# Optimization experiments

Measured on AMD Instinct MI355X. Metric: run time of the kernel, lower is better.

The kernel has to match this reference:

```python
import jax, jax.numpy as jnp
import numpy as np

B, T, E, H = 8, 1024, 1024, 16
D = E // H  # head_dim = 64


def setup_inputs() -> dict:
    key = jax.random.key(0)
    ks = jax.random.split(key, 11)
    s = 1.0 / np.sqrt(E)
    inp = {
        'query': jax.random.normal(ks[0], (B, T, E), jnp.float32),
        'key': jax.random.normal(ks[1], (B, T, E), jnp.float32),
        'value': jax.random.normal(ks[2], (B, T, E), jnp.float32),
        'Wq': jax.random.uniform(ks[3], (E, E), jnp.float32, -s, s),
        'bq': jax.random.uniform(ks[4], (E,), jnp.float32, -s, s),
        'Wk': jax.random.uniform(ks[5], (E, E), jnp.float32, -s, s),
        'bk': jax.random.uniform(ks[6], (E,), jnp.float32, -s, s),
        'Wv': jax.random.uniform(ks[7], (E, E), jnp.float32, -s, s),
        'bv': jax.random.uniform(ks[8], (E,), jnp.float32, -s, s),
        'Wo': jax.random.uniform(ks[9], (E, E), jnp.float32, -s, s),
        'bo': jax.random.uniform(ks[10], (E,), jnp.float32, -s, s),
    }
    return inp


def reference(query, key, value, Wq, bq, Wk, bk, Wv, bv, Wo, bo):
    scale = np.sqrt(D).astype(np.float32)
    # projections: Linear applies x @ W.T + b (torch convention); W shape (out,in)
    q = (query @ Wq.T + bq).reshape(B, T, H, D).transpose(0, 2, 1, 3)  # (B,H,Tq,D)
    k = (key @ Wk.T + bk).reshape(B, T, H, D).transpose(0, 2, 1, 3)    # (B,H,Tk,D)
    v = (value @ Wv.T + bv).reshape(B, T, H, D).transpose(0, 2, 1, 3)  # (B,H,Tk,D)
    scores = jnp.einsum('bhqd,bhkd->bhqk', q, k) / scale
    attn = jax.nn.softmax(scores, axis=-1)  # dropout = identity (eval)
    out = jnp.einsum('bhqk,bhkd->bhqd', attn, v)
    out = out.transpose(0, 2, 1, 3).reshape(B, T, E)
    return out @ Wo.T + bo
```

## Files before the change

### kernel.cpp

```cpp
#include <hip/hip_runtime.h>
#include <stdint.h>

#define BB 8
#define TT 1024
#define EE 1024
#define HH 16
#define DD 64

#define L2E8 0.18033688011112042f

typedef __attribute__((ext_vector_type(8))) __bf16 bf16x8;
typedef __attribute__((ext_vector_type(4))) float f32x4;
typedef __attribute__((ext_vector_type(4))) unsigned short ushort4v;
typedef __attribute__((ext_vector_type(4))) unsigned int uint4v;

__device__ __forceinline__ unsigned short f2bf(float f) {
  unsigned int u = __float_as_uint(f);
  u += 0x7fffu + ((u >> 16) & 1u);
  return (unsigned short)(u >> 16);
}

__device__ __forceinline__ unsigned int pk2t(float a, float b) {
  return __builtin_amdgcn_perm(__float_as_uint(b) + 0x8000u,
                               __float_as_uint(a) + 0x8000u, 0x07060302u);
}

__device__ __forceinline__ f32x4 mfma_16x16x32(bf16x8 a, bf16x8 b, f32x4 c) {
  return __builtin_amdgcn_mfma_f32_16x16x32_bf16(a, b, c, 0, 0, 0);
}

__device__ __forceinline__ void async_ld16(const unsigned short* g, unsigned short* l) {
  __builtin_amdgcn_global_load_lds(
      (const __attribute__((address_space(1))) void*)g,
      (__attribute__((address_space(3))) void*)l, 16, 0, 0);
}

__global__ __launch_bounds__(256) void cast_all(
    const float* __restrict__ xq, const float* __restrict__ xk, const float* __restrict__ xv,
    const float* __restrict__ wq, const float* __restrict__ wk,
    const float* __restrict__ wv, const float* __restrict__ wo,
    unsigned short* __restrict__ ws) {
  int blk = blockIdx.x;
  const float* src; size_t dstoff; int rel;
  if (blk < 4096)       { src = xq; dstoff = 0;        rel = blk; }
  else if (blk < 8192)  { src = xk; dstoff = 8388608;  rel = blk - 4096; }
  else if (blk < 12288) { src = xv; dstoff = 16777216; rel = blk - 8192; }
  else if (blk < 12800) { src = wq; dstoff = 25165824; rel = blk - 12288; }
  else if (blk < 13312) { src = wk; dstoff = 26214400; rel = blk - 12800; }
  else if (blk < 13824) { src = wv; dstoff = 27262976; rel = blk - 13312; }
  else                  { src = wo; dstoff = 28311552; rel = blk - 13824; }
  size_t base = (size_t)rel * 2048 + (size_t)threadIdx.x * 8;
  float4 a = *(const float4*)(src + base);
  float4 b = *(const float4*)(src + base + 4);
  ushort4v o0, o1;
  o0.x = f2bf(a.x); o0.y = f2bf(a.y); o0.z = f2bf(a.z); o0.w = f2bf(a.w);
  o1.x = f2bf(b.x); o1.y = f2bf(b.y); o1.z = f2bf(b.z); o1.w = f2bf(b.w);
  *(ushort4v*)(ws + dstoff + base) = o0;
  *(ushort4v*)(ws + dstoff + base + 4) = o1;
}

__global__ __launch_bounds__(256, 5) void fused_proj(
    const unsigned short* __restrict__ xq, const unsigned short* __restrict__ xk,
    const unsigned short* __restrict__ xv, const unsigned short* __restrict__ wq,
    const unsigned short* __restrict__ wk, const unsigned short* __restrict__ wv,
    const float* __restrict__ bq, const float* __restrict__ bk, const float* __restrict__ bv,
    unsigned short* __restrict__ Qb, unsigned short* __restrict__ Kb,
    unsigned short* __restrict__ Vtb) {
  const int id = blockIdx.x;
  const int tid = threadIdx.x;
  const int wave = tid >> 6, lane = tid & 63;
  const int quad = lane >> 4, l16 = lane & 15;
  const int wr = wave >> 1, wc = wave & 1;

  const unsigned short *A, *W;
  const float* bias;
  int mode, m0, n0;
  size_t zoff = 0;
  if (id < 512) {
    mode = 0; A = xq; W = wq; bias = bq;
    m0 = (id >> 3) * 128; n0 = (id & 7) * 128;
  } else if (id < 1024) {
    int t = id - 512;
    mode = 1; A = xk; W = wk; bias = bk;
    m0 = (t >> 3) * 128; n0 = (t & 7) * 128;
  } else {
    int t = id - 1024;
    int z = t >> 6;
    mode = 2; A = wv; W = xv + (size_t)z * 1048576; bias = bv;
    m0 = ((t >> 3) & 7) * 128; n0 = (t & 7) * 128;
    zoff = (size_t)z * 1048576;
  }

  __shared__ __align__(16) unsigned short As[128 * 64];
  __shared__ __align__(16) unsigned short Bs[128 * 64];

  const unsigned short* Wb = W + (size_t)n0 * 1024;

  f32x4 acc[4][4];
#pragma unroll
  for (int i = 0; i < 4; ++i)
#pragma unroll
    for (int j = 0; j < 4; ++j) acc[i][j] = (f32x4){0.f, 0.f, 0.f, 0.f};

  const int row_s = tid >> 3, c_s = tid & 7;
  const int swl = l16 & 7;
  for (int kt = 0; kt < 16; ++kt) {
    const unsigned short* Akt = A + (size_t)m0 * 1024 + kt * 64;
    const unsigned short* Wkt = Wb + kt * 64;
#pragma unroll
    for (int i = 0; i < 4; ++i) {
      int g = i * 256 + tid;
      int row = row_s + i * 32;
      int gc = c_s ^ (row & 7);
      async_ld16(Akt + (size_t)row * 1024 + gc * 8, As + g * 8);
      async_ld16(Wkt + (size_t)row * 1024 + gc * 8, Bs + g * 8);
    }
    __syncthreads();
#pragma unroll
    for (int ks = 0; ks < 2; ++ks) {
      bf16x8 af[4], bfv[4];
      const int cq = ks * 4 + quad;
      const int sc = cq ^ swl;
#pragma unroll
      for (int i = 0; i < 4; ++i)
        af[i] = *(const bf16x8*)(As + ((wr * 64 + i * 16 + l16) * 8 + sc) * 8);
#pragma unroll
      for (int j = 0; j < 4; ++j)
        bfv[j] = *(const bf16x8*)(Bs + ((wc * 64 + j * 16 + l16) * 8 + sc) * 8);
#pragma unroll
      for (int i = 0; i < 4; ++i)
#pragma unroll
        for (int j = 0; j < 4; ++j) acc[i][j] = mfma_16x16x32(af[i], bfv[j], acc[i][j]);
    }
    __syncthreads();
  }

  if (mode == 2) {
    size_t base = zoff;
    const int nxor = ((((l16 >> 2) + 1) & 2) ? 12 : 0);
#pragma unroll
    for (int i = 0; i < 4; ++i)
#pragma unroll
      for (int r = 0; r < 4; ++r) {
        int m = m0 + wr * 64 + i * 16 + quad * 4 + r;
        float bm = bias[m];
#pragma unroll
        for (int j = 0; j < 4; ++j) {
          int n = (n0 + wc * 64 + j * 16 + l16) ^ nxor;
          Vtb[base + (size_t)m * 1024 + n] = f2bf(acc[i][j][r] + bm);
        }
      }
  } else {
    unsigned short* Out = (mode == 0) ? Qb : Kb;
    const float scale = (mode == 0) ? L2E8 : 1.0f;
#pragma unroll
    for (int j = 0; j < 4; ++j) {
      int n = n0 + wc * 64 + j * 16 + l16;
      float bn = bias[n];
      int h = n >> 6, d = n & 63;
#pragma unroll
      for (int i = 0; i < 4; ++i)
#pragma unroll
        for (int r = 0; r < 4; ++r) {
          int m = m0 + wr * 64 + i * 16 + quad * 4 + r;
          int b = m >> 10, t = m & 1023;
          float v = (acc[i][j][r] + bn) * scale;
          Out[((size_t)((b << 4) + h) * 1024 + t) * 64 + d] = f2bf(v);
        }
    }
  }
}

__global__ __launch_bounds__(256, 4) void gemm_out(
    const unsigned short* __restrict__ A, const unsigned short* __restrict__ Wm,
    const float* __restrict__ bias, float* __restrict__ Cout) {
  const int tid = threadIdx.x;
  const int wave = tid >> 6, lane = tid & 63;
  const int quad = lane >> 4, l16 = lane & 15;
  const int wr = wave >> 1, wc = wave & 1;
  const int n0 = blockIdx.x * 128;
  const int m0 = blockIdx.y * 64;

  __shared__ __align__(16) unsigned short As[64 * 64];
  __shared__ __align__(16) unsigned short Bs[128 * 64];

  const unsigned short* Wb = Wm + (size_t)n0 * 1024;

  f32x4 acc[2][4];
#pragma unroll
  for (int i = 0; i < 2; ++i)
#pragma unroll
    for (int j = 0; j < 4; ++j) acc[i][j] = (f32x4){0.f, 0.f, 0.f, 0.f};

  const int row_s = tid >> 3, c_s = tid & 7;
  const int swl = l16 & 7;
  for (int kt = 0; kt < 16; ++kt) {
    const unsigned short* Akt =
        A + (size_t)(m0 >> 10) * 1048576 + (size_t)kt * 65536 + (size_t)(m0 & 1023) * 64;
    const unsigned short* Wkt = Wb + kt * 64;
#pragma unroll
    for (int i = 0; i < 2; ++i) {
      int row = row_s + i * 32;
      int gc = c_s ^ (row & 7);
      async_ld16(Akt + (size_t)row * 64 + gc * 8, As + (i * 256 + tid) * 8);
    }
#pragma unroll
    for (int i = 0; i < 4; ++i) {
      int row = row_s + i * 32;
      int gc = c_s ^ (row & 7);
      async_ld16(Wkt + (size_t)row * 1024 + gc * 8, Bs + (i * 256 + tid) * 8);
    }
    __syncthreads();
#pragma unroll
    for (int ks = 0; ks < 2; ++ks) {
      bf16x8 af[2], bfv[4];
      const int cq = ks * 4 + quad;
      const int sc = cq ^ swl;
#pragma unroll
      for (int i = 0; i < 2; ++i)
        af[i] = *(const bf16x8*)(As + ((wr * 32 + i * 16 + l16) * 8 + sc) * 8);
#pragma unroll
      for (int j = 0; j < 4; ++j)
        bfv[j] = *(const bf16x8*)(Bs + ((wc * 64 + j * 16 + l16) * 8 + sc) * 8);
#pragma unroll
      for (int i = 0; i < 2; ++i)
#pragma unroll
        for (int j = 0; j < 4; ++j) acc[i][j] = mfma_16x16x32(af[i], bfv[j], acc[i][j]);
    }
    __syncthreads();
  }

#pragma unroll
  for (int j = 0; j < 4; ++j) {
    int n = n0 + wc * 64 + j * 16 + l16;
    float bn = bias[n];
#pragma unroll
    for (int i = 0; i < 2; ++i)
#pragma unroll
      for (int r = 0; r < 4; ++r) {
        int m = m0 + wr * 32 + i * 16 + quad * 4 + r;
        Cout[(size_t)m * 1024 + n] = acc[i][j][r] + bn;
      }
  }
}

__global__ __launch_bounds__(256) void attn(
    const unsigned short* __restrict__ Q,
    const unsigned short* __restrict__ K,
    const unsigned short* __restrict__ Vt,
    unsigned short* __restrict__ O) {
  const int bh = blockIdx.x;
  const int tid = threadIdx.x;
  const int wave = tid >> 6, lane = tid & 63;
  const int quad = lane >> 4, l16 = lane & 15;
  const int q0 = blockIdx.y * 64 + wave * 16;
  const size_t bhTD = (size_t)bh * (TT * DD);
  const unsigned short* Qb = Q + bhTD;
  const unsigned short* Kb = K + bhTD;
  const unsigned short* Vb = Vt + bhTD;

  __shared__ __align__(16) unsigned short Ks[64 * 64];
  __shared__ __align__(16) unsigned short Vs[64 * 64];

  bf16x8 q_lo = *(const bf16x8*)(Qb + (size_t)(q0 + l16) * 64 + quad * 8);
  bf16x8 q_hi = *(const bf16x8*)(Qb + (size_t)(q0 + l16) * 64 + 32 + quad * 8);

  uint4v ou; ou.x = ou.y = ou.z = ou.w = 0x3F803F80u;
  const bf16x8 ones = __builtin_bit_cast(bf16x8, ou);

  f32x4 o_acc[4];
#pragma unroll
  for (int dd = 0; dd < 4; ++dd) o_acc[dd] = (f32x4){0.f, 0.f, 0.f, 0.f};
  f32x4 acc5 = (f32x4){0.f, 0.f, 0.f, 0.f};
  const bool lo_half = (quad < 2);

  const int srow = tid >> 3;
  const int schunk = tid & 7;

  for (int it = 0; it < 16; ++it) {
    const int kv0 = it * 64;
#pragma unroll
    for (int i = 0; i < 2; ++i) {
      int row = srow + i * 32;
      int gc = schunk ^ (row & 7);
      async_ld16(Kb + (size_t)(kv0 + row) * 64 + gc * 8, Ks + (row * 8 + schunk) * 8);
      async_ld16(Vb + (size_t)row * 1024 + kv0 + gc * 8, Vs + (row * 8 + schunk) * 8);
    }
    __syncthreads();

    f32x4 f[4];
#pragma unroll
    for (int c = 0; c < 2; ++c) {
      const int r0 = c * 32 + l16;
      const int r1 = r0 + 16;
      const int sw = r0 & 7;
      bf16x8 k00 = *(const bf16x8*)(Ks + (r0 * 8 + (quad ^ sw)) * 8);
      bf16x8 k01 = *(const bf16x8*)(Ks + (r0 * 8 + ((quad + 4) ^ sw)) * 8);
      bf16x8 k10 = *(const bf16x8*)(Ks + (r1 * 8 + (quad ^ sw)) * 8);
      bf16x8 k11 = *(const bf16x8*)(Ks + (r1 * 8 + ((quad + 4) ^ sw)) * 8);
      f32x4 a = (f32x4){0.f, 0.f, 0.f, 0.f};
      f32x4 b = (f32x4){0.f, 0.f, 0.f, 0.f};
      a = mfma_16x16x32(k00, q_lo, a);
      a = mfma_16x16x32(k01, q_hi, a);
      b = mfma_16x16x32(k10, q_lo, b);
      b = mfma_16x16x32(k11, q_hi, b);
      f[2 * c] = a; f[2 * c + 1] = b;
    }

#pragma unroll
    for (int c = 0; c < 2; ++c) {
      f32x4 f0 = f[2 * c], f1 = f[2 * c + 1];
      float p0 = __builtin_amdgcn_exp2f(f0[0]), p1 = __builtin_amdgcn_exp2f(f0[1]);
      float p2 = __builtin_amdgcn_exp2f(f0[2]), p3 = __builtin_amdgcn_exp2f(f0[3]);
      float p4 = __builtin_amdgcn_exp2f(f1[0]), p5 = __builtin_amdgcn_exp2f(f1[1]);
      float p6 = __builtin_amdgcn_exp2f(f1[2]), p7 = __builtin_amdgcn_exp2f(f1[3]);
      unsigned int u01 = pk2t(p0, p1), u23 = pk2t(p2, p3);
      unsigned int u45 = pk2t(p4, p5), u67 = pk2t(p6, p7);
      unsigned int pu01 = __shfl_xor(u01, 32), pu23 = __shfl_xor(u23, 32);
      unsigned int pu45 = __shfl_xor(u45, 32), pu67 = __shfl_xor(u67, 32);
      uint4v av;
      av.x = lo_half ? u01 : pu45;
      av.y = lo_half ? u23 : pu67;
      av.z = lo_half ? pu01 : u45;
      av.w = lo_half ? pu23 : u67;
      bf16x8 ap = __builtin_bit_cast(bf16x8, av);
      acc5 = mfma_16x16x32(ap, ones, acc5);
#pragma unroll
      for (int dd = 0; dd < 4; ++dd) {
        int vr = dd * 16 + l16;
        bf16x8 bv = *(const bf16x8*)(Vs + (vr * 8 + ((c * 4 + quad) ^ (vr & 7))) * 8);
        o_acc[dd] = mfma_16x16x32(ap, bv, o_acc[dd]);
      }
    }
    __syncthreads();
  }
#pragma unroll
  for (int r = 0; r < 4; ++r) {
    float invr = 1.f / acc5[r];
    int trow = q0 + quad * 4 + r;
#pragma unroll
    for (int dd = 0; dd < 4; ++dd)
      O[bhTD + (size_t)trow * 64 + dd * 16 + l16] = f2bf(o_acc[dd][r] * invr);
  }
}

extern "C" void kernel_launch(void* const* d_in, const int* in_sizes, int n_in,
                              void* d_out, int out_size, void* d_ws, size_t ws_size,
                              hipStream_t stream) {
  const float* xq = (const float*)d_in[0];
  const float* xk = (const float*)d_in[1];
  const float* xv = (const float*)d_in[2];
  const float* Wq = (const float*)d_in[3];
  const float* bq = (const float*)d_in[4];
  const float* Wk = (const float*)d_in[5];
  const float* bk = (const float*)d_in[6];
  const float* Wv = (const float*)d_in[7];
  const float* bv = (const float*)d_in[8];
  const float* Wo = (const float*)d_in[9];
  const float* bo = (const float*)d_in[10];

  unsigned short* ws = (unsigned short*)d_ws;
  unsigned short* xq_b = ws;
  unsigned short* xk_b = ws + 8388608;
  unsigned short* xv_b = ws + 16777216;
  unsigned short* wq_b = ws + 25165824;
  unsigned short* wk_b = ws + 26214400;
  unsigned short* wv_b = ws + 27262976;
  unsigned short* wo_b = ws + 28311552;
  unsigned short* Qbuf = ws + 29360128;
  unsigned short* Kbuf = ws + 37748736;
  unsigned short* Vtb  = ws + 46137344;
  unsigned short* Obuf = ws + 54525952;

  cast_all<<<14336, 256, 0, stream>>>(xq, xk, xv, Wq, Wk, Wv, Wo, ws);

  fused_proj<<<1536, 256, 0, stream>>>(xq_b, xk_b, xv_b, wq_b, wk_b, wv_b,
                                       bq, bk, bv, Qbuf, Kbuf, Vtb);
  attn<<<dim3(128, 16), 256, 0, stream>>>(Qbuf, Kbuf, Vtb, Obuf);
  gemm_out<<<dim3(8, 128), 256, 0, stream>>>(Obuf, wo_b, bo, (float*)d_out);
}
```

Baseline: 338.9 us.

## Double-buffer LDS tiles in projection and output GEMMs with MFMA priority

Both projection and output GEMM kernels now use two LDS buffers per operand and prefetch the next K tile asynchronously while MFMAs run on the current one, leaving one barrier per iteration. MFMA sections are wrapped in s_setprio to favor math waves. Launch-bound occupancy hints drop (5 to 2, 4 to 3) because LDS usage doubles. This trades occupancy-based latency hiding for explicit software pipelining. Whether the async loads into LDS are properly waited on before the barrier depends on async_ld16 and the barrier semantics.

```diff
diff --git a/kernel.cpp b/kernel.cpp
--- a/kernel.cpp
+++ b/kernel.cpp
@@ -59,7 +59,7 @@
   *(ushort4v*)(ws + dstoff + base + 4) = o1;
 }
 
-__global__ __launch_bounds__(256, 5) void fused_proj(
+__global__ __launch_bounds__(256, 2) void fused_proj(
     const unsigned short* __restrict__ xq, const unsigned short* __restrict__ xk,
     const unsigned short* __restrict__ xv, const unsigned short* __restrict__ wq,
     const unsigned short* __restrict__ wk, const unsigned short* __restrict__ wv,
@@ -91,8 +91,8 @@
     zoff = (size_t)z * 1048576;
   }
 
-  __shared__ __align__(16) unsigned short As[128 * 64];
-  __shared__ __align__(16) unsigned short Bs[128 * 64];
+  __shared__ __align__(16) unsigned short As[2][128 * 64];
+  __shared__ __align__(16) unsigned short Bs[2][128 * 64];
 
   const unsigned short* Wb = W + (size_t)n0 * 1024;
 
@@ -104,7 +104,8 @@
 
   const int row_s = tid >> 3, c_s = tid & 7;
   const int swl = l16 & 7;
-  for (int kt = 0; kt < 16; ++kt) {
+
+  auto stage = [&](int sel, int kt) {
     const unsigned short* Akt = A + (size_t)m0 * 1024 + kt * 64;
     const unsigned short* Wkt = Wb + kt * 64;
 #pragma unroll
@@ -112,10 +113,17 @@
       int g = i * 256 + tid;
       int row = row_s + i * 32;
       int gc = c_s ^ (row & 7);
-      async_ld16(Akt + (size_t)row * 1024 + gc * 8, As + g * 8);
-      async_ld16(Wkt + (size_t)row * 1024 + gc * 8, Bs + g * 8);
-    }
-    __syncthreads();
+      async_ld16(Akt + (size_t)row * 1024 + gc * 8, &As[sel][g * 8]);
+      async_ld16(Wkt + (size_t)row * 1024 + gc * 8, &Bs[sel][g * 8]);
+    }
+  };
+
+  stage(0, 0);
+  __syncthreads();
+
+  for (int kt = 0; kt < 16; ++kt) {
+    const int cur = kt & 1;
+    if (kt < 15) stage(cur ^ 1, kt + 1);
 #pragma unroll
     for (int ks = 0; ks < 2; ++ks) {
       bf16x8 af[4], bfv[4];
@@ -123,14 +131,16 @@
       const int sc = cq ^ swl;
 #pragma unroll
       for (int i = 0; i < 4; ++i)
-        af[i] = *(const bf16x8*)(As + ((wr * 64 + i * 16 + l16) * 8 + sc) * 8);
+        af[i] = *(const bf16x8*)(&As[cur][((wr * 64 + i * 16 + l16) * 8 + sc) * 8]);
 #pragma unroll
       for (int j = 0; j < 4; ++j)
-        bfv[j] = *(const bf16x8*)(Bs + ((wc * 64 + j * 16 + l16) * 8 + sc) * 8);
+        bfv[j] = *(const bf16x8*)(&Bs[cur][((wc * 64 + j * 16 + l16) * 8 + sc) * 8]);
+      __builtin_amdgcn_s_setprio(1);
 #pragma unroll
       for (int i = 0; i < 4; ++i)
 #pragma unroll
         for (int j = 0; j < 4; ++j) acc[i][j] = mfma_16x16x32(af[i], bfv[j], acc[i][j]);
+      __builtin_amdgcn_s_setprio(0);
     }
     __syncthreads();
   }
@@ -171,7 +181,7 @@
   }
 }
 
-__global__ __launch_bounds__(256, 4) void gemm_out(
+__global__ __launch_bounds__(256, 3) void gemm_out(
     const unsigned short* __restrict__ A, const unsigned short* __restrict__ Wm,
     const float* __restrict__ bias, float* __restrict__ Cout) {
   const int tid = threadIdx.x;
@@ -181,8 +191,8 @@
   const int n0 = blockIdx.x * 128;
   const int m0 = blockIdx.y * 64;
 
-  __shared__ __align__(16) unsigned short As[64 * 64];
-  __shared__ __align__(16) unsigned short Bs[128 * 64];
+  __shared__ __align__(16) unsigned short As[2][64 * 64];
+  __shared__ __align__(16) unsigned short Bs[2][128 * 64];
 
   const unsigned short* Wb = Wm + (size_t)n0 * 1024;
 
@@ -194,7 +204,8 @@
 
   const int row_s = tid >> 3, c_s = tid & 7;
   const int swl = l16 & 7;
-  for (int kt = 0; kt < 16; ++kt) {
+
+  auto stage = [&](int sel, int kt) {
     const unsigned short* Akt =
         A + (size_t)(m0 >> 10) * 1048576 + (size_t)kt * 65536 + (size_t)(m0 & 1023) * 64;
     const unsigned short* Wkt = Wb + kt * 64;
@@ -202,15 +213,22 @@
     for (int i = 0; i < 2; ++i) {
       int row = row_s + i * 32;
       int gc = c_s ^ (row & 7);
-      async_ld16(Akt + (size_t)row * 64 + gc * 8, As + (i * 256 + tid) * 8);
+      async_ld16(Akt + (size_t)row * 64 + gc * 8, &As[sel][(i * 256 + tid) * 8]);
     }
 #pragma unroll
     for (int i = 0; i < 4; ++i) {
       int row = row_s + i * 32;
       int gc = c_s ^ (row & 7);
-      async_ld16(Wkt + (size_t)row * 1024 + gc * 8, Bs + (i * 256 + tid) * 8);
-    }
-    __syncthreads();
+      async_ld16(Wkt + (size_t)row * 1024 + gc * 8, &Bs[sel][(i * 256 + tid) * 8]);
+    }
+  };
+
+  stage(0, 0);
+  __syncthreads();
+
+  for (int kt = 0; kt < 16; ++kt) {
+    const int cur = kt & 1;
+    if (kt < 15) stage(cur ^ 1, kt + 1);
 #pragma unroll
     for (int ks = 0; ks < 2; ++ks) {
       bf16x8 af[2], bfv[4];
@@ -218,14 +236,16 @@
       const int sc = cq ^ swl;
 #pragma unroll
       for (int i = 0; i < 2; ++i)
-        af[i] = *(const bf16x8*)(As + ((wr * 32 + i * 16 + l16) * 8 + sc) * 8);
+        af[i] = *(const bf16x8*)(&As[cur][((wr * 32 + i * 16 + l16) * 8 + sc) * 8]);
 #pragma unroll
       for (int j = 0; j < 4; ++j)
-        bfv[j] = *(const bf16x8*)(Bs + ((wc * 64 + j * 16 + l16) * 8 + sc) * 8);
+        bfv[j] = *(const bf16x8*)(&Bs[cur][((wc * 64 + j * 16 + l16) * 8 + sc) * 8]);
+      __builtin_amdgcn_s_setprio(1);
 #pragma unroll
       for (int i = 0; i < 2; ++i)
 #pragma unroll
         for (int j = 0; j < 4; ++j) acc[i][j] = mfma_16x16x32(af[i], bfv[j], acc[i][j]);
+      __builtin_amdgcn_s_setprio(0);
     }
     __syncthreads();
   }
```

Measured after the change: 312.7 us. 1.08x faster.
